# Kernel tuning notes

Measured on AMD Instinct MI355X. Metric: run time of the kernel, lower is better.

The kernel has to match this reference:

```python
import jax, jax.numpy as jnp
import numpy as np

D_IN = 3
HID = 256
N_BRANCH = 8
SKIP_IN = (4,)
CSG_TREE = [0, 1, [2, 3], [4, 5, [6, 7]]]
FLAG_CONVEX = True
BETA = 100.0
N_POINTS = 100000

# layer dims: [3, 256*7, 8]; layer whose OUTPUT feeds a skip layer emits 256-3=253
_DIMS = [D_IN] + [HID] * 7 + [N_BRANCH]


def _layer_out_dim(layer):
    if (layer + 1) in SKIP_IN:
        return _DIMS[layer + 1] - D_IN
    return _DIMS[layer + 1]


def setup_inputs() -> dict:
    key = jax.random.key(0)
    keys = jax.random.split(key, 20)
    inp = {"x": jax.random.normal(keys[0], (N_POINTS, D_IN), dtype=jnp.float32)}
    n_layers = len(_DIMS) - 1  # 8 linear layers
    for layer in range(n_layers):
        in_d = _DIMS[layer]
        out_d = _layer_out_dim(layer)
        kw = jax.random.fold_in(keys[1], layer)
        if layer == n_layers - 1:  # geometric init of last layer
            W = (np.sqrt(np.pi) / np.sqrt(in_d)
                 + 1e-5 * jax.random.normal(kw, (in_d, out_d), dtype=jnp.float32))
            b = -1.0 * jnp.ones((out_d,), dtype=jnp.float32)
        else:
            W = (np.sqrt(2.0) / np.sqrt(out_d)) * jax.random.normal(
                kw, (in_d, out_d), dtype=jnp.float32)
            b = jnp.zeros((out_d,), dtype=jnp.float32)
        inp[f"W{layer}"] = W
        inp[f"b{layer}"] = b
    return inp


def _softplus_beta(x):
    return jax.nn.softplus(BETA * x) / BETA


def _csg_combine(vals, ops, cvx_flag):
    # hard CSG tree: one-hot matmul == column gather; recursion is static (trace time)
    idxs = [v for v in ops if not isinstance(v, list)]
    cols = [vals[:, jnp.array(idxs)]]
    for v in ops:
        if isinstance(v, list):
            cols.append(_csg_combine(vals, v, not cvx_flag))
    m = jnp.concatenate(cols, axis=1)
    red = jnp.max if cvx_flag else jnp.min
    return red(m, axis=1, keepdims=True)


def _forward(x, Ws, bs):
    inp = x
    h = x
    n_layers = len(Ws)
    inv_sqrt2 = np.float32(1.0 / np.sqrt(2.0))
    for layer in range(n_layers):
        if layer in SKIP_IN:
            h = jnp.concatenate([h, inp], axis=-1) * inv_sqrt2
        h = h @ Ws[layer] + bs[layer]
        if layer < n_layers - 1:
            h = _softplus_beta(h)
    branch_vals = h  # [N, n_branch]
    hcsg = _csg_combine(branch_vals, CSG_TREE, FLAG_CONVEX)  # [N, 1]
    return jnp.concatenate([hcsg, branch_vals], axis=1)  # flag_output == 0


def reference(x, W0, b0, W1, b1, W2, b2, W3, b3, W4, b4, W5, b5, W6, b6, W7, b7):
    Ws = [W0, W1, W2, W3, W4, W5, W6, W7]
    bs = [b0, b1, b2, b3, b4, b5, b6, b7]
    return _forward(x, Ws, bs)
```

## Files before the change

### kernel.cpp

```cpp
#include <hip/hip_runtime.h>
#include <hip/hip_bf16.h>


using bf16x8 = __attribute__((ext_vector_type(8))) __bf16;
using f32x4  = __attribute__((ext_vector_type(4))) float;

#define LDA 264

#define OFFW0 0
#define OFFW1 8192
#define OFFW2 73728
#define OFFW3 139264
#define OFFW4 204800
#define OFFW5 270336
#define OFFW6 335872
#define OFFW7 401408
#define WSB_BYTE_OFF 811008
#define OFFB7 1792

#define SCALE_T2 144.26950408889634f
#define INV_SQRT2 0.70710678118654752f
#define LN2_100 0.0069314718055994531f

__device__ __forceinline__ float fast_exp2(float x) {
#if __has_builtin(__builtin_amdgcn_exp2f)
    return __builtin_amdgcn_exp2f(x);
#else
    return exp2f(x);
#endif
}
__device__ __forceinline__ float fast_log2(float x) {
#if __has_builtin(__builtin_amdgcn_logf)
    return __builtin_amdgcn_logf(x);
#else
    return log2f(x);
#endif
}

__device__ __forceinline__ float softplus_t2(float t2) {
    float e = fast_exp2(-fabsf(t2));
    float l = fast_log2(1.0f + e);
    return fmaxf(t2, 0.0f) + l;
}

__device__ __forceinline__ unsigned short bf16_rne(float f) {
    unsigned int u = __float_as_uint(f);
    unsigned int r = u + 0x7FFFu + ((u >> 16) & 1u);
    return (unsigned short)(r >> 16);
}

template <int KK, int MODE>
__device__ __forceinline__ void layer_mm(
    const unsigned short* __restrict__ wfrag,
    const float* __restrict__ bias,
    unsigned short* act, const float* xst,
    int wave, int lane)
{
    const int quad = lane >> 4;
    const int l15  = lane & 15;

    f32x4 acc[2][4];
#pragma unroll
    for (int i = 0; i < 2; ++i) {
        const int chb = (wave * 2 + i) * 16 + quad * 4;
        const float4 b4 = *(const float4*)(bias + chb);
#pragma unroll
        for (int nt = 0; nt < 4; ++nt)
            acc[i][nt] = f32x4{b4.x, b4.y, b4.z, b4.w};
    }

    const unsigned short* wbase = wfrag + (wave * 2 * KK * 64 + lane) * 8;

#pragma unroll
    for (int kk = 0; kk < KK; ++kk) {
        bf16x8 bfr[4];
#pragma unroll
        for (int nt = 0; nt < 4; ++nt)
            bfr[nt] = *(const bf16x8*)(act + (nt * 16 + l15) * LDA + kk * 32 + quad * 8);
#pragma unroll
        for (int i = 0; i < 2; ++i) {
            bf16x8 afr = *(const bf16x8*)(wbase + (i * KK + kk) * 512);
#pragma unroll
            for (int nt = 0; nt < 4; ++nt)
                acc[i][nt] = __builtin_amdgcn_mfma_f32_16x16x32_bf16(afr, bfr[nt], acc[i][nt], 0, 0, 0);
        }
    }

    __syncthreads();

#pragma unroll
    for (int i = 0; i < 2; ++i) {
        const int chb = (wave * 2 + i) * 16 + quad * 4;
#pragma unroll
        for (int nt = 0; nt < 4; ++nt) {
            const int pt = nt * 16 + l15;
            float vv[4];
#pragma unroll
            for (int r = 0; r < 4; ++r) {
                float s = softplus_t2(acc[i][nt][r]);
                if (MODE == 1) {
                    const int ch = chb + r;
                    if (ch >= 253)
                        s = xst[pt * 4 + (ch - 253)];
                }
                vv[r] = s;
            }
            __hip_bfloat162 p01 = __float22bfloat162_rn(float2{vv[0], vv[1]});
            __hip_bfloat162 p23 = __float22bfloat162_rn(float2{vv[2], vv[3]});
            uint2 pk;
            pk.x = *(unsigned int*)&p01;
            pk.y = *(unsigned int*)&p23;
            *(uint2*)(act + pt * LDA + chb) = pk;
        }
    }

    __syncthreads();
}

__global__ __launch_bounds__(512, 4)
void nhrep_main(const float* __restrict__ x, float* __restrict__ out,
                const unsigned short* __restrict__ wsW,
                const float* __restrict__ wsB, int npts)
{
    __shared__ unsigned short act[64 * LDA];
    __shared__ float xst[64 * 4];
    const int tid  = threadIdx.x;
    const int wave = tid >> 6, lane = tid & 63;
    const int quad = lane >> 4, l15 = lane & 15;
    const int base_pt = blockIdx.x * 64;

    for (int i = tid; i < 64 * 32; i += 512) {
        const int pt = i >> 5, ch = i & 31;
        const int ptg = base_pt + pt;
        float v = 0.0f;
        if (ch < 3 && ptg < npts) v = x[ptg * 3 + ch];
        act[pt * LDA + ch] = bf16_rne(v);
        if (ch < 4) xst[pt * 4 + ch] = (ch < 3) ? v : 0.0f;
    }
    __syncthreads();

    layer_mm<1, 0>(wsW + OFFW0, wsB + 0 * 256, act, xst, wave, lane);
    layer_mm<8, 0>(wsW + OFFW1, wsB + 1 * 256, act, xst, wave, lane);
    layer_mm<8, 0>(wsW + OFFW2, wsB + 2 * 256, act, xst, wave, lane);
    layer_mm<8, 1>(wsW + OFFW3, wsB + 3 * 256, act, xst, wave, lane);
    layer_mm<8, 0>(wsW + OFFW4, wsB + 4 * 256, act, xst, wave, lane);
    layer_mm<8, 0>(wsW + OFFW5, wsB + 5 * 256, act, xst, wave, lane);
    layer_mm<8, 0>(wsW + OFFW6, wsB + 6 * 256, act, xst, wave, lane);

    if (wave < 4) {
        const float4 b4 = *(const float4*)(wsB + OFFB7 + quad * 4);
        f32x4 acc = f32x4{b4.x, b4.y, b4.z, b4.w};
        const unsigned short* w7 = wsW + OFFW7;
#pragma unroll
        for (int kk = 0; kk < 8; ++kk) {
            bf16x8 bfr = *(const bf16x8*)(act + (wave * 16 + l15) * LDA + kk * 32 + quad * 8);
            bf16x8 afr = *(const bf16x8*)(w7 + (kk * 64 + lane) * 8);
            acc = __builtin_amdgcn_mfma_f32_16x16x32_bf16(afr, bfr, acc, 0, 0, 0);
        }
        float u0 = __shfl(acc[0], l15 + 16);
        float u1 = __shfl(acc[1], l15 + 16);
        float u2 = __shfl(acc[2], l15 + 16);
        float u3 = __shfl(acc[3], l15 + 16);
        if (quad == 0) {
            const int ptg = base_pt + wave * 16 + l15;
            if (ptg < npts) {
                const float v0 = acc[0], v1 = acc[1], v2 = acc[2], v3 = acc[3];
                const float v4 = u0, v5 = u1, v6 = u2, v7 = u3;
                const float m23   = fminf(v2, v3);
                const float m67   = fmaxf(v6, v7);
                const float m4567 = fminf(fminf(v4, v5), m67);
                const float h     = fmaxf(fmaxf(v0, v1), fmaxf(m23, m4567));
                float* o = out + (long)ptg * 9;
                o[0] = h;
                o[1] = v0; o[2] = v1; o[3] = v2; o[4] = v3;
                o[5] = v4; o[6] = v5; o[7] = v6; o[8] = v7;
            }
        }
    }
}

struct PackArgs {
    const float* W[8];
    const float* b[8];
};

#define TOTAL_FRAGS 50688
#define TOTAL_BIAS  1808

__global__ void prepack_all(PackArgs args, unsigned short* __restrict__ dstW,
                            float* __restrict__ dstB)
{
    const int t = blockIdx.x * blockDim.x + threadIdx.x;
    const int FB[9]  = {0, 1024, 9216, 17408, 25600, 33792, 41984, 50176, 50688};
    const int KKs[8] = {1, 8, 8, 8, 8, 8, 8, 8};
    const int ind[8] = {3, 256, 256, 256, 256, 256, 256, 256};
    const int outd[8]= {256, 256, 256, 253, 256, 256, 256, 8};

    if (t < TOTAL_FRAGS) {
        int l = 0;
        while (t >= FB[l + 1]) ++l;
        const int f    = t - FB[l];
        const int lane = f & 63;
        const int kk   = (f >> 6) % KKs[l];
        const int mt   = f / (64 * KKs[l]);
        const int o    = mt * 16 + (lane & 15);
        const int kb   = kk * 32 + (lane >> 4) * 8;
        const float* W = args.W[l];
        const int in_d = ind[l], out_d = outd[l];

        unsigned short v[8];
#pragma unroll
        for (int j = 0; j < 8; ++j) {
            const int k = kb + j;
            float w = 0.0f;
            if (k < in_d && o < out_d) {
                float sc = 1.0f;
                if (l == 0) sc = SCALE_T2;
                else if (l == 4) sc = (k < 253) ? INV_SQRT2 : (SCALE_T2 * INV_SQRT2);
                else if (l == 7) sc = LN2_100;
                w = W[k * out_d + o] * sc;
            }
            unsigned int u = __float_as_uint(w);
            v[j] = (unsigned short)((u + 0x7FFFu + ((u >> 16) & 1u)) >> 16);
        }
        uint4 p;
        p.x = (unsigned int)v[0] | ((unsigned int)v[1] << 16);
        p.y = (unsigned int)v[2] | ((unsigned int)v[3] << 16);
        p.z = (unsigned int)v[4] | ((unsigned int)v[5] << 16);
        p.w = (unsigned int)v[6] | ((unsigned int)v[7] << 16);
        *(uint4*)(dstW + (long)t * 8) = p;
    } else if (t < TOTAL_FRAGS + TOTAL_BIAS) {
        const int u = t - TOTAL_FRAGS;
        const int l = (u < 1792) ? (u >> 8) : 7;
        const int idx = (l < 7) ? (u & 255) : (u - 1792);
        const float sc = (l < 7) ? SCALE_T2 : 1.0f;
        dstB[u] = (idx < outd[l]) ? args.b[l][idx] * sc : 0.0f;
    }
}

extern "C" void kernel_launch(void* const* d_in, const int* in_sizes, int n_in,
                              void* d_out, int out_size, void* d_ws, size_t ws_size,
                              hipStream_t stream)
{
    const float* x = (const float*)d_in[0];
    unsigned short* wsW = (unsigned short*)d_ws;
    float* wsB = (float*)((char*)d_ws + WSB_BYTE_OFF);

    PackArgs pa;
    for (int l = 0; l < 8; ++l) {
        pa.W[l] = (const float*)d_in[1 + 2 * l];
        pa.b[l] = (const float*)d_in[2 + 2 * l];
    }
    const int ptot = TOTAL_FRAGS + TOTAL_BIAS;
    prepack_all<<<(ptot + 255) / 256, 256, 0, stream>>>(pa, wsW, wsB);

    const int npts = in_sizes[0] / 3;
    const int nblk = (npts + 63) / 64;
    nhrep_main<<<nblk, 512, 0, stream>>>(x, (float*)d_out, wsW, wsB, npts);
}
```

Before: 203.6 us.

## Ping-pong activation buffers and split tail into half-size blocks

Double-buffers the shared activation tile (read from one buffer, write to the other) so the barrier between the MFMA loop and the epilogue writeback can be dropped, leaving one barrier per layer. It also processes the last ~16K points with 32-point blocks instead of 64 to even out the final wave of blocks across CUs. This doubles shared memory per block, which may lower occupancy, and the small blocks use the MFMA units less efficiently.

```diff
diff --git a/kernel.cpp b/kernel.cpp
--- a/kernel.cpp
+++ b/kernel.cpp
@@ -49,23 +49,23 @@
     return (unsigned short)(r >> 16);
 }
 
-template <int KK, int MODE>
+template <int KK, int MODE, int NT>
 __device__ __forceinline__ void layer_mm(
     const unsigned short* __restrict__ wfrag,
     const float* __restrict__ bias,
-    unsigned short* act, const float* xst,
-    int wave, int lane)
+    const unsigned short* src, unsigned short* dst,
+    const float* xst, int wave, int lane)
 {
     const int quad = lane >> 4;
     const int l15  = lane & 15;
 
-    f32x4 acc[2][4];
+    f32x4 acc[2][NT];
 #pragma unroll
     for (int i = 0; i < 2; ++i) {
         const int chb = (wave * 2 + i) * 16 + quad * 4;
         const float4 b4 = *(const float4*)(bias + chb);
 #pragma unroll
-        for (int nt = 0; nt < 4; ++nt)
+        for (int nt = 0; nt < NT; ++nt)
             acc[i][nt] = f32x4{b4.x, b4.y, b4.z, b4.w};
     }
 
@@ -73,26 +73,24 @@
 
 #pragma unroll
     for (int kk = 0; kk < KK; ++kk) {
-        bf16x8 bfr[4];
-#pragma unroll
-        for (int nt = 0; nt < 4; ++nt)
-            bfr[nt] = *(const bf16x8*)(act + (nt * 16 + l15) * LDA + kk * 32 + quad * 8);
+        bf16x8 bfr[NT];
+#pragma unroll
+        for (int nt = 0; nt < NT; ++nt)
+            bfr[nt] = *(const bf16x8*)(src + (nt * 16 + l15) * LDA + kk * 32 + quad * 8);
 #pragma unroll
         for (int i = 0; i < 2; ++i) {
             bf16x8 afr = *(const bf16x8*)(wbase + (i * KK + kk) * 512);
 #pragma unroll
-            for (int nt = 0; nt < 4; ++nt)
+            for (int nt = 0; nt < NT; ++nt)
                 acc[i][nt] = __builtin_amdgcn_mfma_f32_16x16x32_bf16(afr, bfr[nt], acc[i][nt], 0, 0, 0);
         }
     }
-
-    __syncthreads();
 
 #pragma unroll
     for (int i = 0; i < 2; ++i) {
         const int chb = (wave * 2 + i) * 16 + quad * 4;
 #pragma unroll
-        for (int nt = 0; nt < 4; ++nt) {
+        for (int nt = 0; nt < NT; ++nt) {
             const int pt = nt * 16 + l15;
             float vv[4];
 #pragma unroll
@@ -110,50 +108,48 @@
             uint2 pk;
             pk.x = *(unsigned int*)&p01;
             pk.y = *(unsigned int*)&p23;
-            *(uint2*)(act + pt * LDA + chb) = pk;
+            *(uint2*)(dst + pt * LDA + chb) = pk;
         }
     }
 
     __syncthreads();
 }
 
-__global__ __launch_bounds__(512, 4)
-void nhrep_main(const float* __restrict__ x, float* __restrict__ out,
-                const unsigned short* __restrict__ wsW,
-                const float* __restrict__ wsB, int npts)
-{
-    __shared__ unsigned short act[64 * LDA];
-    __shared__ float xst[64 * 4];
-    const int tid  = threadIdx.x;
+template <int NT>
+__device__ __forceinline__ void run_net(
+    const float* __restrict__ x, float* __restrict__ out,
+    const unsigned short* __restrict__ wsW, const float* __restrict__ wsB,
+    unsigned short* actA, unsigned short* actB, float* xst,
+    int base_pt, int npts, int tid)
+{
     const int wave = tid >> 6, lane = tid & 63;
     const int quad = lane >> 4, l15 = lane & 15;
-    const int base_pt = blockIdx.x * 64;
-
-    for (int i = tid; i < 64 * 32; i += 512) {
+
+    for (int i = tid; i < NT * 16 * 32; i += 512) {
         const int pt = i >> 5, ch = i & 31;
         const int ptg = base_pt + pt;
         float v = 0.0f;
         if (ch < 3 && ptg < npts) v = x[ptg * 3 + ch];
-        act[pt * LDA + ch] = bf16_rne(v);
+        actA[pt * LDA + ch] = bf16_rne(v);
         if (ch < 4) xst[pt * 4 + ch] = (ch < 3) ? v : 0.0f;
     }
     __syncthreads();
 
-    layer_mm<1, 0>(wsW + OFFW0, wsB + 0 * 256, act, xst, wave, lane);
-    layer_mm<8, 0>(wsW + OFFW1, wsB + 1 * 256, act, xst, wave, lane);
-    layer_mm<8, 0>(wsW + OFFW2, wsB + 2 * 256, act, xst, wave, lane);
-    layer_mm<8, 1>(wsW + OFFW3, wsB + 3 * 256, act, xst, wave, lane);
-    layer_mm<8, 0>(wsW + OFFW4, wsB + 4 * 256, act, xst, wave, lane);
-    layer_mm<8, 0>(wsW + OFFW5, wsB + 5 * 256, act, xst, wave, lane);
-    layer_mm<8, 0>(wsW + OFFW6, wsB + 6 * 256, act, xst, wave, lane);
-
-    if (wave < 4) {
+    layer_mm<1, 0, NT>(wsW + OFFW0, wsB + 0 * 256, actA, actB, xst, wave, lane);
+    layer_mm<8, 0, NT>(wsW + OFFW1, wsB + 1 * 256, actB, actA, xst, wave, lane);
+    layer_mm<8, 0, NT>(wsW + OFFW2, wsB + 2 * 256, actA, actB, xst, wave, lane);
+    layer_mm<8, 1, NT>(wsW + OFFW3, wsB + 3 * 256, actB, actA, xst, wave, lane);
+    layer_mm<8, 0, NT>(wsW + OFFW4, wsB + 4 * 256, actA, actB, xst, wave, lane);
+    layer_mm<8, 0, NT>(wsW + OFFW5, wsB + 5 * 256, actB, actA, xst, wave, lane);
+    layer_mm<8, 0, NT>(wsW + OFFW6, wsB + 6 * 256, actA, actB, xst, wave, lane);
+
+    if (wave < NT) {
         const float4 b4 = *(const float4*)(wsB + OFFB7 + quad * 4);
         f32x4 acc = f32x4{b4.x, b4.y, b4.z, b4.w};
         const unsigned short* w7 = wsW + OFFW7;
 #pragma unroll
         for (int kk = 0; kk < 8; ++kk) {
-            bf16x8 bfr = *(const bf16x8*)(act + (wave * 16 + l15) * LDA + kk * 32 + quad * 8);
+            bf16x8 bfr = *(const bf16x8*)(actB + (wave * 16 + l15) * LDA + kk * 32 + quad * 8);
             bf16x8 afr = *(const bf16x8*)(w7 + (kk * 64 + lane) * 8);
             acc = __builtin_amdgcn_mfma_f32_16x16x32_bf16(afr, bfr, acc, 0, 0, 0);
         }
@@ -179,6 +175,23 @@
     }
 }
 
+__global__ __launch_bounds__(512, 4)
+void nhrep_main(const float* __restrict__ x, float* __restrict__ out,
+                const unsigned short* __restrict__ wsW,
+                const float* __restrict__ wsB, int npts, int nbig)
+{
+    __shared__ unsigned short actA[64 * LDA];
+    __shared__ unsigned short actB[64 * LDA];
+    __shared__ float xst[64 * 4];
+    const int b = blockIdx.x;
+    if (b < nbig) {
+        run_net<4>(x, out, wsW, wsB, actA, actB, xst, b * 64, npts, threadIdx.x);
+    } else {
+        run_net<2>(x, out, wsW, wsB, actA, actB, xst,
+                   nbig * 64 + (b - nbig) * 32, npts, threadIdx.x);
+    }
+}
+
 struct PackArgs {
     const float* W[8];
     const float* b[8];
@@ -255,6 +268,16 @@
     prepack_all<<<(ptot + 255) / 256, 256, 0, stream>>>(pa, wsW, wsB);
 
     const int npts = in_sizes[0] / 3;
-    const int nblk = (npts + 63) / 64;
-    nhrep_main<<<nblk, 512, 0, stream>>>(x, (float*)d_out, wsW, wsB, npts);
-}
+    int nbig, nsmall;
+    const int tail_pts = 16384;
+    if (npts > tail_pts) {
+        nbig = (npts - tail_pts + 63) / 64;
+        const int base_small = nbig * 64;
+        nsmall = (npts - base_small + 31) / 32;
+    } else {
+        nbig = 0;
+        nsmall = (npts + 31) / 32;
+    }
+    nhrep_main<<<nbig + nsmall, 512, 0, stream>>>(x, (float*)d_out, wsW, wsB,
+                                                  npts, nbig);
+}
```

Result: faster. 193.9 us (-4.7%).
